# Performance work log

Hardware: AMD Instinct MI355X
Metric: run time of the kernel (lower is better)

The kernel has to match this reference:

```python
import jax, jax.numpy as jnp
import numpy as np

THRESHOLD = 0.5

def setup_inputs() -> dict:
    key = jax.random.key(0)
    x = jax.random.normal(key, (32, 2048, 1024), dtype=jnp.float32)
    return {"x": x}

def reference(x) -> jnp.ndarray:
    # x: [B, S, D]
    B, S, D = x.shape
    x_centered = x - jnp.mean(x, axis=1, keepdims=True)          # [B, S, D]
    # per-sample covariance: [B, D, D]
    cov = jnp.einsum('bsd,bse->bde', x_centered, x_centered) / (S - 1)
    std = jnp.sqrt(jnp.diagonal(cov, axis1=1, axis2=2))          # [B, D]
    corr = cov / (std[:, :, None] * std[:, None, :])             # [B, D, D]
    mask = jnp.abs(corr) > THRESHOLD                             # [B, D, D]
    eye = jnp.eye(D, dtype=bool)
    mask = mask & ~eye                                           # zero the diagonal
    # torch semantics: output[b, :, j] = 0 for every masked (b, i, j)
    col_kill = jnp.any(mask, axis=1)                             # [B, D]
    return x * (~col_kill)[:, None, :].astype(x.dtype)
```

## Files before the change

kernel.cpp:

```cpp
#include <hip/hip_runtime.h>
#include <stdint.h>

#define B_ 32
#define S_ 2048
#define D_ 1024

typedef __attribute__((ext_vector_type(16))) float f32x16;

__device__ __forceinline__ void async_copy16(const void* g, void* l) {
  __builtin_amdgcn_global_load_lds(
      (const __attribute__((address_space(1))) uint32_t*)g,
      (__attribute__((address_space(3))) uint32_t*)l, 16, 0, 0);
}

__device__ __forceinline__ int row_off(int m, int ch) {
  return m * 128 + ((ch ^ (m & 7)) << 4);
}

__global__ __launch_bounds__(256) void prepass_kernel(const float* __restrict__ x,
                                                      uint8_t* __restrict__ xt,
                                                      float2* __restrict__ part) {
  __shared__ float s_s[256 * 4];
  __shared__ float s_q[256 * 4];
  int dt = blockIdx.x;
  int slab = blockIdx.y;
  int b = blockIdx.z;
  int t = threadIdx.x;
  int q = t & 31;
  int e = t >> 5;
  int g = e >> 1, bh = e & 1;

  const float* xb = x + ((size_t)b * S_ + (size_t)slab * 128 + g * 32 + bh * 8) * D_ +
                    dt * 128 + q * 4;
  float4 r[16];
#pragma unroll
  for (int j = 0; j < 8; ++j) r[j] = *(const float4*)(xb + (size_t)j * D_);
#pragma unroll
  for (int j = 0; j < 8; ++j) r[8 + j] = *(const float4*)(xb + (size_t)(16 + j) * D_);

  uint8_t* img = xt + (((size_t)b * 8 + dt) * 16 + slab) * 16384;
#pragma unroll
  for (int c = 0; c < 4; ++c) {
    float v[16];
#pragma unroll
    for (int j = 0; j < 16; ++j) v[j] = ((const float*)&r[j])[c];
    float ps = 0.f, pq = 0.f;
#pragma unroll
    for (int j = 0; j < 16; ++j) { ps += v[j]; pq += v[j] * v[j]; }
    s_s[t * 4 + c] = ps;
    s_q[t * 4 + c] = pq;
    uint32_t w0 = 0, w1 = 0, w2 = 0, w3 = 0;
    w0 = __builtin_amdgcn_cvt_pk_fp8_f32(v[0], v[1], w0, false);
    w0 = __builtin_amdgcn_cvt_pk_fp8_f32(v[2], v[3], w0, true);
    w1 = __builtin_amdgcn_cvt_pk_fp8_f32(v[4], v[5], w1, false);
    w1 = __builtin_amdgcn_cvt_pk_fp8_f32(v[6], v[7], w1, true);
    w2 = __builtin_amdgcn_cvt_pk_fp8_f32(v[8], v[9], w2, false);
    w2 = __builtin_amdgcn_cvt_pk_fp8_f32(v[10], v[11], w2, true);
    w3 = __builtin_amdgcn_cvt_pk_fp8_f32(v[12], v[13], w3, false);
    w3 = __builtin_amdgcn_cvt_pk_fp8_f32(v[14], v[15], w3, true);
    int m = 4 * q + c;
    *(uint4*)(img + row_off(m, (g << 1) | bh)) = make_uint4(w0, w1, w2, w3);
  }
  __syncthreads();
  if (t < 128) {
    int m = t, qq = m >> 2, cc = m & 3;
    float ss = 0.f, sq = 0.f;
#pragma unroll
    for (int ee = 0; ee < 8; ++ee) {
      ss += s_s[(qq + 32 * ee) * 4 + cc];
      sq += s_q[(qq + 32 * ee) * 4 + cc];
    }
    part[(size_t)slab * 32768 + b * 1024 + dt * 128 + m] = make_float2(ss, sq);
  }
}

__global__ void finalize_kernel(const float2* __restrict__ part,
                                float* __restrict__ meanB,
                                float* __restrict__ stdB) {
  int i = blockIdx.x * 256 + threadIdx.x;
  float s = 0.f, qv = 0.f;
#pragma unroll
  for (int sl = 0; sl < 16; ++sl) {
    float2 p = part[(size_t)sl * 32768 + i];
    s += p.x;
    qv += p.y;
  }
  float m = s * (1.0f / (float)S_);
  float var = (qv - s * m) * (1.0f / (float)(S_ - 1));
  meanB[i] = m;
  stdB[i] = sqrtf(fmaxf(var, 0.f));
}

__global__ __launch_bounds__(256) void gram_kernel(const uint8_t* __restrict__ xt,
                                                   const float* __restrict__ meanB,
                                                   const float* __restrict__ stdB,
                                                   int* __restrict__ colkill) {
  __shared__ uint8_t smA[16384];
  __shared__ uint8_t smB[16384];
  int b = blockIdx.y;
  int p = blockIdx.x;
  int i = 0;
  while (p >= 8 - i) { p -= 8 - i; ++i; }
  int j = i + p;

  int tid = threadIdx.x;
  int lane = tid & 63, wave = tid >> 6;
  int wm = wave & 1, wn = wave >> 1;
  int l31 = lane & 31, half = lane >> 5;

  f32x16 acc[2][2];
#pragma unroll
  for (int a = 0; a < 2; ++a)
#pragma unroll
    for (int c = 0; c < 2; ++c)
#pragma unroll
      for (int r = 0; r < 16; ++r) acc[a][c][r] = 0.f;

  const uint8_t* gA = xt + ((size_t)b * 8 + i) * 262144;
  const uint8_t* gB = xt + ((size_t)b * 8 + j) * 262144;
  bool diag = (i == j);

  for (int sl = 0; sl < 16; ++sl) {
    __syncthreads();
    const uint8_t* srcA = gA + (size_t)sl * 16384;
    for (int c = wave; c < 16; c += 4)
      async_copy16(srcA + c * 1024 + lane * 16, (void*)(smA + c * 1024));
    if (!diag) {
      const uint8_t* srcB = gB + (size_t)sl * 16384;
      for (int c = wave; c < 16; c += 4)
        async_copy16(srcB + c * 1024 + lane * 16, (void*)(smB + c * 1024));
    }
    __syncthreads();

    const uint8_t* bA = smA;
    const uint8_t* bB = diag ? smA : smB;
#pragma unroll
    for (int g = 0; g < 4; ++g) {
      ulonglong2 a0 = *(const ulonglong2*)(bA + row_off(wm * 64 + l31, (g << 1) | half));
      ulonglong2 a1 = *(const ulonglong2*)(bA + row_off(wm * 64 + 32 + l31, (g << 1) | half));
      ulonglong2 b0 = *(const ulonglong2*)(bB + row_off(wn * 64 + l31, (g << 1) | half));
      ulonglong2 b1 = *(const ulonglong2*)(bB + row_off(wn * 64 + 32 + l31, (g << 1) | half));
      acc[0][0] = __builtin_amdgcn_mfma_f32_32x32x16_fp8_fp8((long)a0.x, (long)b0.x, acc[0][0], 0, 0, 0);
      acc[0][1] = __builtin_amdgcn_mfma_f32_32x32x16_fp8_fp8((long)a0.x, (long)b1.x, acc[0][1], 0, 0, 0);
      acc[1][0] = __builtin_amdgcn_mfma_f32_32x32x16_fp8_fp8((long)a1.x, (long)b0.x, acc[1][0], 0, 0, 0);
      acc[1][1] = __builtin_amdgcn_mfma_f32_32x32x16_fp8_fp8((long)a1.x, (long)b1.x, acc[1][1], 0, 0, 0);
      acc[0][0] = __builtin_amdgcn_mfma_f32_32x32x16_fp8_fp8((long)a0.y, (long)b0.y, acc[0][0], 0, 0, 0);
      acc[0][1] = __builtin_amdgcn_mfma_f32_32x32x16_fp8_fp8((long)a0.y, (long)b1.y, acc[0][1], 0, 0, 0);
      acc[1][0] = __builtin_amdgcn_mfma_f32_32x32x16_fp8_fp8((long)a1.y, (long)b0.y, acc[1][0], 0, 0, 0);
      acc[1][1] = __builtin_amdgcn_mfma_f32_32x32x16_fp8_fp8((long)a1.y, (long)b1.y, acc[1][1], 0, 0, 0);
    }
  }

  const float* mb = meanB + b * D_;
  const float* sb = stdB + b * D_;
#pragma unroll
  for (int t = 0; t < 2; ++t) {
#pragma unroll
    for (int u = 0; u < 2; ++u) {
      int e = j * 128 + wn * 64 + u * 32 + l31;
      float me = mb[e], se05 = 0.5f * sb[e];
#pragma unroll
      for (int r = 0; r < 16; ++r) {
        int row = half * 4 + (r & 3) + 8 * (r >> 2);
        int d = i * 128 + wm * 64 + t * 32 + row;
        float cov = (acc[t][u][r] - (float)S_ * mb[d] * me) * (1.0f / (float)(S_ - 1));
        if (d != e && fabsf(cov) > se05 * sb[d]) {
          atomicOr(colkill + b * D_ + e, 1);
          atomicOr(colkill + b * D_ + d, 1);
        }
      }
    }
  }
}

__global__ void apply_kernel(const float* __restrict__ x,
                             const int* __restrict__ colkill,
                             float* __restrict__ out) {
  size_t idx = (size_t)blockIdx.x * 256 + threadIdx.x;
  const float4 v = ((const float4*)x)[idx];
  size_t e0 = idx * 4;
  int d = (int)(e0 & (D_ - 1));
  int b = (int)(e0 >> 21);
  const int4 k = *(const int4*)(colkill + b * D_ + d);
  float4 o;
  o.x = k.x ? 0.f : v.x;
  o.y = k.y ? 0.f : v.y;
  o.z = k.z ? 0.f : v.z;
  o.w = k.w ? 0.f : v.w;
  ((float4*)out)[idx] = o;
}

extern "C" void kernel_launch(void* const* d_in, const int* in_sizes, int n_in,
                              void* d_out, int out_size, void* d_ws, size_t ws_size,
                              hipStream_t stream) {
  const float* x = (const float*)d_in[0];
  float* out = (float*)d_out;

  uint8_t* xt = (uint8_t*)d_out;

  float2* part = (float2*)d_ws;
  float* meanB = (float*)((uint8_t*)d_ws + (16 * 32768) * sizeof(float2));
  float* stdB = meanB + 32768;
  int* colkill = (int*)(stdB + 32768);

  hipMemsetAsync(colkill, 0, 32768 * sizeof(int), stream);
  prepass_kernel<<<dim3(8, 16, 32), 256, 0, stream>>>(x, xt, part);
  finalize_kernel<<<128, 256, 0, stream>>>(part, meanB, stdB);
  gram_kernel<<<dim3(36, 32), 256, 0, stream>>>(xt, meanB, stdB, colkill);
  apply_kernel<<<65536, 256, 0, stream>>>(x, colkill, out);
}
```

Measured before the change: 571.1 us.

## Copy input to output during prepass and zero only killed columns

Result: faster. 529.3 us (-7.3%).

```diff
diff --git a/kernel.cpp b/kernel.cpp
--- a/kernel.cpp
+++ b/kernel.cpp
@@ -17,9 +17,11 @@
   return m * 128 + ((ch ^ (m & 7)) << 4);
 }
 
+template <bool COPY>
 __global__ __launch_bounds__(256) void prepass_kernel(const float* __restrict__ x,
                                                       uint8_t* __restrict__ xt,
-                                                      float2* __restrict__ part) {
+                                                      float2* __restrict__ part,
+                                                      float* __restrict__ out) {
   __shared__ float s_s[256 * 4];
   __shared__ float s_q[256 * 4];
   int dt = blockIdx.x;
@@ -30,13 +32,22 @@
   int e = t >> 5;
   int g = e >> 1, bh = e & 1;
 
-  const float* xb = x + ((size_t)b * S_ + (size_t)slab * 128 + g * 32 + bh * 8) * D_ +
-                    dt * 128 + q * 4;
+  const size_t base = ((size_t)b * S_ + (size_t)slab * 128 + g * 32 + bh * 8) * D_ +
+                      dt * 128 + q * 4;
+  const float* xb = x + base;
   float4 r[16];
 #pragma unroll
   for (int j = 0; j < 8; ++j) r[j] = *(const float4*)(xb + (size_t)j * D_);
 #pragma unroll
   for (int j = 0; j < 8; ++j) r[8 + j] = *(const float4*)(xb + (size_t)(16 + j) * D_);
+
+  if (COPY) {
+    float* ob = out + base;
+#pragma unroll
+    for (int j = 0; j < 8; ++j) *(float4*)(ob + (size_t)j * D_) = r[j];
+#pragma unroll
+    for (int j = 0; j < 8; ++j) *(float4*)(ob + (size_t)(16 + j) * D_) = r[8 + j];
+  }
 
   uint8_t* img = xt + (((size_t)b * 8 + dt) * 16 + slab) * 16384;
 #pragma unroll
@@ -190,22 +201,46 @@
   ((float4*)out)[idx] = o;
 }
 
+__global__ __launch_bounds__(256) void zerocol_kernel(const int* __restrict__ colkill,
+                                                      float* __restrict__ out) {
+  int bd = blockIdx.x * 256 + threadIdx.x;
+  if (colkill[bd] == 0) return;
+  int b = bd >> 10, d = bd & (D_ - 1);
+  float* p = out + (size_t)b * S_ * D_ + d;
+#pragma unroll 8
+  for (int s = 0; s < S_; ++s) p[(size_t)s * D_] = 0.f;
+}
+
 extern "C" void kernel_launch(void* const* d_in, const int* in_sizes, int n_in,
                               void* d_out, int out_size, void* d_ws, size_t ws_size,
                               hipStream_t stream) {
   const float* x = (const float*)d_in[0];
   float* out = (float*)d_out;
 
-  uint8_t* xt = (uint8_t*)d_out;
-
-  float2* part = (float2*)d_ws;
-  float* meanB = (float*)((uint8_t*)d_ws + (16 * 32768) * sizeof(float2));
-  float* stdB = meanB + 32768;
-  int* colkill = (int*)(stdB + 32768);
-
-  hipMemsetAsync(colkill, 0, 32768 * sizeof(int), stream);
-  prepass_kernel<<<dim3(8, 16, 32), 256, 0, stream>>>(x, xt, part);
-  finalize_kernel<<<128, 256, 0, stream>>>(part, meanB, stdB);
-  gram_kernel<<<dim3(36, 32), 256, 0, stream>>>(xt, meanB, stdB, colkill);
-  apply_kernel<<<65536, 256, 0, stream>>>(x, colkill, out);
-}
+  const size_t need = ((size_t)69 << 20);
+  if (ws_size >= need) {
+    uint8_t* xt = (uint8_t*)d_ws;
+    float2* part = (float2*)((uint8_t*)d_ws + ((size_t)64 << 20));
+    float* meanB = (float*)((uint8_t*)d_ws + ((size_t)68 << 20));
+    float* stdB = meanB + 32768;
+    int* colkill = (int*)(stdB + 32768);
+
+    hipMemsetAsync(colkill, 0, 32768 * sizeof(int), stream);
+    prepass_kernel<true><<<dim3(8, 16, 32), 256, 0, stream>>>(x, xt, part, out);
+    finalize_kernel<<<128, 256, 0, stream>>>(part, meanB, stdB);
+    gram_kernel<<<dim3(36, 32), 256, 0, stream>>>(xt, meanB, stdB, colkill);
+    zerocol_kernel<<<128, 256, 0, stream>>>(colkill, out);
+  } else {
+    uint8_t* xt = (uint8_t*)d_out;
+    float2* part = (float2*)d_ws;
+    float* meanB = (float*)((uint8_t*)d_ws + (16 * 32768) * sizeof(float2));
+    float* stdB = meanB + 32768;
+    int* colkill = (int*)(stdB + 32768);
+
+    hipMemsetAsync(colkill, 0, 32768 * sizeof(int), stream);
+    prepass_kernel<false><<<dim3(8, 16, 32), 256, 0, stream>>>(x, xt, part, nullptr);
+    finalize_kernel<<<128, 256, 0, stream>>>(part, meanB, stdB);
+    gram_kernel<<<dim3(36, 32), 256, 0, stream>>>(xt, meanB, stdB, colkill);
+    apply_kernel<<<65536, 256, 0, stream>>>(x, colkill, out);
+  }
+}
```
